# Kernel optimization log

Hardware: AMD Instinct MI355X
Metric: run time of the kernel (lower is better)

Reference implementation:

```python
import jax, jax.numpy as jnp
import numpy as np

LOSS_WEIGHT = 1.0
GAMMA = 0.8


def setup_inputs() -> dict:
    key = jax.random.key(0)
    L, B, K, H, W = 4, 64, 17, 256, 256
    k1, k2, k3 = jax.random.split(key, 3)
    pred_flows = jax.random.normal(k1, (L, B, 2, H, W), dtype=jnp.float32)
    # frame-0 keypoints: distinct row per keypoint (no duplicate scatter targets),
    # random column -> deterministic equivalence with the torch sequential writes
    y0 = jnp.broadcast_to((jnp.arange(K, dtype=jnp.int32) * (H // K)), (B, K))
    x0 = jax.random.randint(k2, (B, K), 0, W, dtype=jnp.int32)
    kps0 = jnp.stack([x0, y0], axis=-1)              # [B,K,2] (x,y)
    kps1 = jax.random.randint(k3, (B, K, 2), 0, W, dtype=jnp.int32)
    kps = jnp.stack([kps0, kps1], axis=1)            # [B,2,K,2]
    return {"pred_flows": pred_flows, "kps": kps}


def reference(pred_flows, kps):
    L, B, C, H, W = pred_flows.shape
    x0 = kps[:, 0, :, 0]
    y0 = kps[:, 0, :, 1]
    x1 = kps[:, 1, :, 0]
    y1 = kps[:, 1, :, 1]
    dx = (x1 - x0).astype(pred_flows.dtype)          # [B,K]
    dy = (y1 - y0).astype(pred_flows.dtype)
    b = jnp.arange(B)[:, None]                       # [B,1] broadcasts vs [B,K]
    gt_flow = jnp.zeros((B, C, H, W), dtype=pred_flows.dtype)
    gt_flow = gt_flow.at[b, 0, y0, x0].set(dx)
    gt_flow = gt_flow.at[b, 1, y0, x0].set(dy)
    # mask where flow vector norm > 0
    mask = (jnp.sqrt(gt_flow[:, 0] ** 2 + gt_flow[:, 1] ** 2) > 0)  # [B,H,W]
    maskf = mask.astype(pred_flows.dtype)[:, None]   # [B,1,H,W]
    # F.mse_loss averages over all 2*N selected elements
    denom = jnp.maximum(jnp.sum(maskf) * C, 1.0)
    loss = jnp.zeros((), dtype=pred_flows.dtype)
    for i in range(L):
        sse = jnp.sum(((pred_flows[i] - gt_flow) ** 2) * maskf)
        loss = loss + (sse / denom) * (GAMMA ** (L - 1 - i))
    return loss * LOSS_WEIGHT
```

## Files before the change

### kernel.cpp

```cpp
#include <hip/hip_runtime.h>


#define LL 4
#define BB 64
#define KK 17
#define HH 256
#define WW 256
#define GAMMA 0.8f

__global__ __launch_bounds__(1024) void KeypointFlowLoss_28767690949028_kernel(
    const float* __restrict__ pred,
    const int*   __restrict__ kps,
    float*       __restrict__ out)
{
    const int tid = threadIdx.x;
    const float wts[LL] = {GAMMA * GAMMA * GAMMA, GAMMA * GAMMA, GAMMA, 1.0f};

    float wsse = 0.0f;
    float cnt  = 0.0f;

    for (int idx = tid; idx < BB * KK; idx += 1024) {
        const int b = idx / KK;
        const int k = idx - b * KK;
        const int* k0 = kps + ((b * 2 + 0) * KK + k) * 2;
        const int* k1 = kps + ((b * 2 + 1) * KK + k) * 2;
        const int x0 = k0[0], y0 = k0[1];
        const int x1 = k1[0], y1 = k1[1];
        const int dxi = x1 - x0, dyi = y1 - y0;
        if (dxi != 0 || dyi != 0) {
            cnt += 1.0f;
            const float dx = (float)dxi, dy = (float)dyi;
            const size_t base = (size_t)b * (2 * HH * WW) + (size_t)y0 * WW + x0;
#pragma unroll
            for (int i = 0; i < LL; ++i) {
                const size_t o = (size_t)i * (BB * 2 * HH * WW) + base;
                const float p0 = pred[o];
                const float p1 = pred[o + HH * WW];
                const float e0 = p0 - dx, e1 = p1 - dy;
                wsse += wts[i] * (e0 * e0 + e1 * e1);
            }
        }
    }

#pragma unroll
    for (int off = 32; off > 0; off >>= 1) {
        wsse += __shfl_down(wsse, off, 64);
        cnt  += __shfl_down(cnt,  off, 64);
    }

    __shared__ float s_wsse[16], s_cnt[16];
    const int wave = tid >> 6;
    const int lane = tid & 63;
    if (lane == 0) { s_wsse[wave] = wsse; s_cnt[wave] = cnt; }
    __syncthreads();

    if (wave == 0) {
        float v = (lane < 16) ? s_wsse[lane] : 0.0f;
        float c = (lane < 16) ? s_cnt[lane]  : 0.0f;
#pragma unroll
        for (int off = 8; off > 0; off >>= 1) {
            v += __shfl_down(v, off, 64);
            c += __shfl_down(c, off, 64);
        }
        if (lane == 0) {
            const float denom = fmaxf(c * 2.0f, 1.0f);
            out[0] = v / denom;
        }
    }
}

extern "C" void kernel_launch(void* const* d_in, const int* in_sizes, int n_in,
                              void* d_out, int out_size, void* d_ws, size_t ws_size,
                              hipStream_t stream) {
    const float* pred = (const float*)d_in[0];
    const int*   kps  = (const int*)d_in[1];
    float*       out  = (float*)d_out;
    (void)in_sizes; (void)n_in; (void)out_size; (void)d_ws; (void)ws_size;
    KeypointFlowLoss_28767690949028_kernel<<<1, 1024, 0, stream>>>(pred, kps, out);
}
```

Baseline: 178.9 us.

## Split keypoint gather across many blocks with a second reduction kernel

Replaces the single-block kernel with a multi-block gather kernel in which each thread loads one predicted flow element for one keypoint, level and channel. Per-block partial sums go to workspace, and a small second kernel does the final reduction and normalization. This exposes more memory-level parallelism for the scattered gathers, at the cost of an extra kernel launch and a workspace round-trip.

```diff
diff --git a/kernel.cpp b/kernel.cpp
--- a/kernel.cpp
+++ b/kernel.cpp
@@ -8,38 +8,39 @@
 #define WW 256
 #define GAMMA 0.8f
 
-__global__ __launch_bounds__(1024) void KeypointFlowLoss_28767690949028_kernel(
+#define NKP (BB * KK)
+#define NTH (NKP * LL * 2)
+#define BLK 256
+#define NBLK (NTH / BLK)
+
+__global__ __launch_bounds__(BLK) void kfl_gather(
     const float* __restrict__ pred,
     const int*   __restrict__ kps,
-    float*       __restrict__ out)
+    float*       __restrict__ ws)
 {
-    const int tid = threadIdx.x;
-    const float wts[LL] = {GAMMA * GAMMA * GAMMA, GAMMA * GAMMA, GAMMA, 1.0f};
+    const int t  = blockIdx.x * BLK + threadIdx.x;
+    const int kp = t >> 3;
+    const int r  = t & 7;
 
-    float wsse = 0.0f;
-    float cnt  = 0.0f;
+    const int b = kp / KK;
+    const int k = kp - b * KK;
+    const int* k0 = kps + ((b * 2 + 0) * KK + k) * 2;
+    const int* k1 = kps + ((b * 2 + 1) * KK + k) * 2;
+    const int x0 = k0[0], y0 = k0[1];
+    const int dxi = k1[0] - x0, dyi = k1[1] - y0;
 
-    for (int idx = tid; idx < BB * KK; idx += 1024) {
-        const int b = idx / KK;
-        const int k = idx - b * KK;
-        const int* k0 = kps + ((b * 2 + 0) * KK + k) * 2;
-        const int* k1 = kps + ((b * 2 + 1) * KK + k) * 2;
-        const int x0 = k0[0], y0 = k0[1];
-        const int x1 = k1[0], y1 = k1[1];
-        const int dxi = x1 - x0, dyi = y1 - y0;
-        if (dxi != 0 || dyi != 0) {
-            cnt += 1.0f;
-            const float dx = (float)dxi, dy = (float)dyi;
-            const size_t base = (size_t)b * (2 * HH * WW) + (size_t)y0 * WW + x0;
-#pragma unroll
-            for (int i = 0; i < LL; ++i) {
-                const size_t o = (size_t)i * (BB * 2 * HH * WW) + base;
-                const float p0 = pred[o];
-                const float p1 = pred[o + HH * WW];
-                const float e0 = p0 - dx, e1 = p1 - dy;
-                wsse += wts[i] * (e0 * e0 + e1 * e1);
-            }
-        }
+    float wsse = 0.0f, cnt = 0.0f;
+    if (dxi | dyi) {
+        const int i = r >> 1, c = r & 1;
+        const float wts[LL] = {GAMMA * GAMMA * GAMMA, GAMMA * GAMMA, GAMMA, 1.0f};
+        const float d = c ? (float)dyi : (float)dxi;
+        const size_t o = (size_t)i * (BB * 2 * HH * WW)
+                       + (size_t)b * (2 * HH * WW)
+                       + (size_t)c * (HH * WW)
+                       + (size_t)y0 * WW + (size_t)x0;
+        const float e = pred[o] - d;
+        wsse = wts[i] * e * e;
+        cnt  = (r == 0) ? 1.0f : 0.0f;
     }
 
 #pragma unroll
@@ -48,24 +49,32 @@
         cnt  += __shfl_down(cnt,  off, 64);
     }
 
-    __shared__ float s_wsse[16], s_cnt[16];
-    const int wave = tid >> 6;
-    const int lane = tid & 63;
-    if (lane == 0) { s_wsse[wave] = wsse; s_cnt[wave] = cnt; }
+    __shared__ float sw[4], sc[4];
+    const int wave = threadIdx.x >> 6;
+    const int lane = threadIdx.x & 63;
+    if (lane == 0) { sw[wave] = wsse; sc[wave] = cnt; }
     __syncthreads();
 
-    if (wave == 0) {
-        float v = (lane < 16) ? s_wsse[lane] : 0.0f;
-        float c = (lane < 16) ? s_cnt[lane]  : 0.0f;
+    if (threadIdx.x == 0) {
+        ws[blockIdx.x]        = sw[0] + sw[1] + sw[2] + sw[3];
+        ws[NBLK + blockIdx.x] = sc[0] + sc[1] + sc[2] + sc[3];
+    }
+}
+
+__global__ __launch_bounds__(64) void kfl_final(
+    const float* __restrict__ ws,
+    float*       __restrict__ out)
+{
+    const int lane = threadIdx.x;
+    float v = (lane < NBLK) ? ws[lane]        : 0.0f;
+    float c = (lane < NBLK) ? ws[NBLK + lane] : 0.0f;
 #pragma unroll
-        for (int off = 8; off > 0; off >>= 1) {
-            v += __shfl_down(v, off, 64);
-            c += __shfl_down(c, off, 64);
-        }
-        if (lane == 0) {
-            const float denom = fmaxf(c * 2.0f, 1.0f);
-            out[0] = v / denom;
-        }
+    for (int off = 32; off > 0; off >>= 1) {
+        v += __shfl_down(v, off, 64);
+        c += __shfl_down(c, off, 64);
+    }
+    if (lane == 0) {
+        out[0] = v / fmaxf(c * 2.0f, 1.0f);
     }
 }
 
@@ -75,6 +84,9 @@
     const float* pred = (const float*)d_in[0];
     const int*   kps  = (const int*)d_in[1];
     float*       out  = (float*)d_out;
-    (void)in_sizes; (void)n_in; (void)out_size; (void)d_ws; (void)ws_size;
-    KeypointFlowLoss_28767690949028_kernel<<<1, 1024, 0, stream>>>(pred, kps, out);
+    float*       ws   = (float*)d_ws;
+    (void)in_sizes; (void)n_in; (void)out_size; (void)ws_size;
+
+    kfl_gather<<<NBLK, BLK, 0, stream>>>(pred, kps, ws);
+    kfl_final<<<1, 64, 0, stream>>>(ws, out);
 }
```

Result: faster. 160.8 us (-10.1%).
